# Kernel tuning notes

Hardware: AMD Instinct MI355X
Metric: run time of the kernel (lower is better)

## Reference

```python
import jax, jax.numpy as jnp
import numpy as np

TEMPERATURE = 8.0  # sqrt(head_dim=64)


def setup_inputs() -> dict:
    key = jax.random.key(0)
    kq, kk, kv, km = jax.random.split(key, 4)
    B, S, D = 16, 2048, 64
    q = jax.random.normal(kq, (B, S, D), dtype=jnp.float32)
    k = jax.random.normal(kk, (B, S, D), dtype=jnp.float32)
    v = jax.random.normal(kv, (B, S, D), dtype=jnp.float32)
    mask = jax.random.randint(km, (B, S, S), 0, 2).astype(jnp.bool_)
    return {"q": q, "k": k, "v": v, "mask": mask}


def reference(q, k, v, mask):
    # latent = q @ k^T / temperature  -> [B, Sq, Sk]
    latent = jnp.einsum('bqd,bkd->bqk', q, k) / TEMPERATURE
    # NOTE: the original fills masked positions with 1e-9 (NOT -inf); keep faithful.
    latent = jnp.where(mask, jnp.float32(1e-9), latent)
    attn = jax.nn.softmax(latent, axis=-1)
    return jnp.einsum('bqk,bkd->bqd', attn, v)
```

## Files before the change

kernel.cpp:

```cpp
#include <hip/hip_runtime.h>
#include <hip/hip_bf16.h>

#define BB 16
#define SS 2048
#define DD 64

typedef __attribute__((ext_vector_type(8)))  unsigned short ushort8;
typedef __attribute__((ext_vector_type(8)))  __bf16 bf16x8;
typedef __attribute__((ext_vector_type(16))) float f32x16;

static __device__ __forceinline__ unsigned short f2bf(float x) {
    return __builtin_bit_cast(unsigned short, __float2bfloat16(x));
}
static __device__ __forceinline__ unsigned pk2(float a, float b) {
    return (unsigned)f2bf(a) | ((unsigned)f2bf(b) << 16);
}
union F4 { float4 v; float a[4]; };

__global__ __launch_bounds__(256, 4)
void sdpa_mfma_kernel(const float* __restrict__ Q, const float* __restrict__ K,
                      const float* __restrict__ V, const unsigned int* __restrict__ M,
                      float* __restrict__ O) {
    __shared__ __align__(16) char smem[37120];
    char* Ks = smem;
    char* Vs = smem + 16384;
    char* Ms = smem + 32768;
    char* Qs = smem + 32768;
    float* red  = (float*)smem;
    float* denx = (float*)(smem + 32768);

    const int t    = threadIdx.x;
    const int lane = t & 63;
    const int l31  = lane & 31;
    const int half = lane >> 5;
    const int kh   = t >> 6;
    const int b    = blockIdx.y;
    const int q0   = blockIdx.x * 32;

    const float* Kg = K + (size_t)b * SS * DD;
    const float* Vg = V + (size_t)b * SS * DD;
    const unsigned int* Mg = M + (size_t)b * SS * SS + (size_t)q0 * SS;

    {
        const int sr = t >> 3, sc = t & 7;
        const float* src = Q + ((size_t)b * SS + q0 + sr) * DD + sc * 8;
        F4 f0, f1; f0.v = *(const float4*)src; f1.v = *(const float4*)(src + 4);
        ushort8 u;
        #pragma unroll
        for (int e = 0; e < 4; e++) {
            u[e]     = f2bf(f0.a[e] * 0.125f);
            u[e + 4] = f2bf(f1.a[e] * 0.125f);
        }
        *(ushort8*)(Qs + sr * 128 + ((sc ^ (sr & 7)) * 16)) = u;
    }
    __syncthreads();

    const int qrow = l31;
    bf16x8 bq[4];
    #pragma unroll
    for (int dc = 0; dc < 4; dc++)
        bq[dc] = __builtin_bit_cast(bf16x8, *(const ushort8*)(
            Qs + qrow * 128 + (((2 * dc + half) ^ (qrow & 7)) * 16)));
    __syncthreads();

    f32x16 On0, On1;
    #pragma unroll
    for (int i = 0; i < 16; i++) { On0[i] = 0.f; On1[i] = 0.f; }
    float den_acc = 0.f;

    const int krow = 32 * kh + l31;
    const int d0v  = (t & 15) * 4;
    const int kkb  = (t >> 4) * 4;

    for (int kt = 0; kt < SS / 128; ++kt) {
        #pragma unroll
        for (int j = 0; j < 4; j++) {
            const int idx = 2 * t + 512 * j;
            const int row = idx >> 4;
            const int g   = (idx & 15) >> 1;
            const float* src = Kg + (size_t)(kt * 128) * DD + (size_t)idx * 4;
            F4 fa, fb; fa.v = *(const float4*)src; fb.v = *(const float4*)(src + 4);
            ushort8 u;
            #pragma unroll
            for (int e = 0; e < 4; e++) { u[e] = f2bf(fa.a[e]); u[e + 4] = f2bf(fb.a[e]); }
            *(ushort8*)(Ks + row * 128 + ((g ^ (row & 7)) * 16)) = u;
        }
        #pragma unroll
        for (int it2 = 0; it2 < 2; it2++) {
            const int kk = kkb + 64 * it2;
            const float* src = Vg + (size_t)(kt * 128 + kk) * DD + d0v;
            F4 r0, r1, r2, r3;
            r0.v = *(const float4*)(src);
            r1.v = *(const float4*)(src + DD);
            r2.v = *(const float4*)(src + 2 * DD);
            r3.v = *(const float4*)(src + 3 * DD);
            #pragma unroll
            for (int e = 0; e < 4; e++) {
                const int d = d0v + e;
                const uint2 wv = make_uint2(pk2(r0.a[e], r1.a[e]), pk2(r2.a[e], r3.a[e]));
                *(uint2*)(Vs + d * 256 + (((kk >> 3) ^ (d & 15)) * 16) + (kk & 7) * 2) = wv;
            }
        }
        {
            const int sr = t >> 3, sc = t & 7;
            const unsigned int* Mw = Mg + (size_t)sr * SS + kt * 128 + sc * 16;
            unsigned wd[4];
            #pragma unroll
            for (int g = 0; g < 4; g++) {
                const uint4 u = *(const uint4*)(Mw + 4 * g);
                wd[g] = (u.x ? 1u : 0u) | (u.y ? 0x100u : 0u) |
                        (u.z ? 0x10000u : 0u) | (u.w ? 0x1000000u : 0u);
            }
            *(uint2*)(Ms + sr * 136 + sc * 16)     = make_uint2(wd[0], wd[1]);
            *(uint2*)(Ms + sr * 136 + sc * 16 + 8) = make_uint2(wd[2], wd[3]);
        }
        __syncthreads();

        f32x16 S;
        #pragma unroll
        for (int i = 0; i < 16; i++) S[i] = 0.f;
        #pragma unroll
        for (int dc = 0; dc < 4; dc++) {
            bf16x8 ak = __builtin_bit_cast(bf16x8, *(const ushort8*)(
                Ks + krow * 128 + (((2 * dc + half) ^ (krow & 7)) * 16)));
            S = __builtin_amdgcn_mfma_f32_32x32x16_bf16(ak, bq[dc], S, 0, 0, 0);
        }

        float p[16];
        #pragma unroll
        for (int g = 0; g < 4; g++) {
            const unsigned mw = *(const unsigned*)(Ms + qrow * 136 + 32 * kh + 8 * g + 4 * half);
            #pragma unroll
            for (int e = 0; e < 4; e++) {
                const float ev = __expf(S[4 * g + e]);
                const float pv = ((mw >> (8 * e)) & 0xffu) ? 1.0f : ev;
                p[4 * g + e] = pv;
                den_acc += pv;
            }
        }

        #pragma unroll
        for (int s2 = 0; s2 < 2; s2++) {
            const unsigned o0 = pk2(p[8 * s2 + 0], p[8 * s2 + 1]);
            const unsigned o1 = pk2(p[8 * s2 + 2], p[8 * s2 + 3]);
            const unsigned o2 = pk2(p[8 * s2 + 4], p[8 * s2 + 5]);
            const unsigned o3 = pk2(p[8 * s2 + 6], p[8 * s2 + 7]);
            const unsigned s0 = half ? o0 : o2;
            const unsigned s1 = half ? o1 : o3;
            const unsigned r0 = (unsigned)__shfl_xor((int)s0, 32, 64);
            const unsigned r1 = (unsigned)__shfl_xor((int)s1, 32, 64);
            uint4 bu;
            bu.x = half ? r0 : o0;
            bu.y = half ? r1 : o1;
            bu.z = half ? o2 : r0;
            bu.w = half ? o3 : r1;
            const bf16x8 bp = __builtin_bit_cast(bf16x8, bu);
            #pragma unroll
            for (int dc = 0; dc < 2; dc++) {
                const int vrow = 32 * dc + l31;
                bf16x8 av = __builtin_bit_cast(bf16x8, *(const ushort8*)(
                    Vs + vrow * 256 + (((4 * kh + 2 * s2 + half) ^ (vrow & 15)) * 16)));
                if (dc == 0) On0 = __builtin_amdgcn_mfma_f32_32x32x16_bf16(av, bp, On0, 0, 0, 0);
                else         On1 = __builtin_amdgcn_mfma_f32_32x32x16_bf16(av, bp, On1, 0, 0, 0);
            }
        }
        __syncthreads();
    }

    const float den_tot = den_acc + __shfl_xor(den_acc, 32, 64);

    __syncthreads();
    if (kh != 0) {
        #pragma unroll
        for (int dc = 0; dc < 2; dc++)
            #pragma unroll
            for (int g = 0; g < 4; g++) {
                const f32x16& Oc = dc ? On1 : On0;
                float4 st;
                st.x = Oc[4 * g + 0]; st.y = Oc[4 * g + 1];
                st.z = Oc[4 * g + 2]; st.w = Oc[4 * g + 3];
                *(float4*)((char*)red + (kh - 1) * 8192 + (dc * 4 + g) * 1024 + lane * 16) = st;
            }
        if (lane < 32) denx[kh * 32 + l31] = den_tot;
    }
    __syncthreads();
    if (kh == 0) {
        const float inv = 1.0f / (den_tot + denx[32 + l31] + denx[64 + l31] + denx[96 + l31]);
        float* Og = O + ((size_t)b * SS + q0 + qrow) * DD;
        #pragma unroll
        for (int dc = 0; dc < 2; dc++)
            #pragma unroll
            for (int g = 0; g < 4; g++) {
                const f32x16& Oc = dc ? On1 : On0;
                float4 st;
                st.x = Oc[4 * g + 0]; st.y = Oc[4 * g + 1];
                st.z = Oc[4 * g + 2]; st.w = Oc[4 * g + 3];
                #pragma unroll
                for (int w2 = 0; w2 < 3; w2++) {
                    const float4 pr = *(const float4*)((char*)red + w2 * 8192 +
                                                       (dc * 4 + g) * 1024 + lane * 16);
                    st.x += pr.x; st.y += pr.y; st.z += pr.z; st.w += pr.w;
                }
                st.x *= inv; st.y *= inv; st.z *= inv; st.w *= inv;
                *(float4*)(Og + 32 * dc + 8 * g + 4 * half) = st;
            }
    }
}

extern "C" void kernel_launch(void* const* d_in, const int* in_sizes, int n_in,
                              void* d_out, int out_size, void* d_ws, size_t ws_size,
                              hipStream_t stream) {
    const float* q = (const float*)d_in[0];
    const float* k = (const float*)d_in[1];
    const float* v = (const float*)d_in[2];
    const unsigned int* m = (const unsigned int*)d_in[3];
    float* out = (float*)d_out;

    dim3 grid(SS / 32, BB);
    sdpa_mfma_kernel<<<grid, 256, 0, stream>>>(q, k, v, m, out);
}
```

Before: 394.4 us.

## Prepack the whole mask block into a bitmask before the key loop

The mask for the block's 32 query rows is now streamed once up front, with a one-row-ahead register prefetch, and compressed into a 1-bit-per-key table in shared memory. The per-tile mask staging and byte-packing inside the key loop are removed, and each lane reads a single 32-bit word per tile. This takes mask traffic out of the main loop's critical path and shrinks the per-tile shared-memory footprint. The cost is a serialized prologue of 32 dependent row loads, slightly more shared memory (40 KB), which may reduce occupancy, and the removal of a barrier before the reduction scratch reuses shared memory.

```diff
diff --git a/kernel.cpp b/kernel.cpp
--- a/kernel.cpp
+++ b/kernel.cpp
@@ -4,6 +4,7 @@
 #define BB 16
 #define SS 2048
 #define DD 64
+#define NTB 16
 
 typedef __attribute__((ext_vector_type(8)))  unsigned short ushort8;
 typedef __attribute__((ext_vector_type(8)))  __bf16 bf16x8;
@@ -21,13 +22,11 @@
 void sdpa_mfma_kernel(const float* __restrict__ Q, const float* __restrict__ K,
                       const float* __restrict__ V, const unsigned int* __restrict__ M,
                       float* __restrict__ O) {
-    __shared__ __align__(16) char smem[37120];
-    char* Ks = smem;
-    char* Vs = smem + 16384;
-    char* Ms = smem + 32768;
-    char* Qs = smem + 32768;
-    float* red  = (float*)smem;
-    float* denx = (float*)(smem + 32768);
+    __shared__ __align__(16) char smem[40960];
+    char* Ks   = smem;
+    char* Vs   = smem + 16384;
+    char* Qs   = smem + 32768;
+    char* Bits = smem + 32768;
 
     const int t    = threadIdx.x;
     const int lane = t & 63;
@@ -39,7 +38,12 @@
 
     const float* Kg = K + (size_t)b * SS * DD;
     const float* Vg = V + (size_t)b * SS * DD;
-    const unsigned int* Mg = M + (size_t)b * SS * SS + (size_t)q0 * SS;
+    const unsigned int* Mblk = M + (size_t)b * SS * SS + (size_t)q0 * SS;
+
+    const int kw  = t >> 2;
+    const int bsh = 8 * (t & 3);
+    uint4 c0 = *(const uint4*)(Mblk + 8 * t);
+    uint4 c1 = *(const uint4*)(Mblk + 8 * t + 4);
 
     {
         const int sr = t >> 3, sc = t & 7;
@@ -63,6 +67,23 @@
             Qs + qrow * 128 + (((2 * dc + half) ^ (qrow & 7)) * 16)));
     __syncthreads();
 
+    for (int s = 0; s < 32; ++s) {
+        const int sn = (s + 1 < 32) ? s + 1 : 31;
+        const uint4 n0 = *(const uint4*)(Mblk + (size_t)sn * SS + 8 * t);
+        const uint4 n1 = *(const uint4*)(Mblk + (size_t)sn * SS + 8 * t + 4);
+        unsigned byt = (unsigned)(c0.x != 0u)        | ((unsigned)(c0.y != 0u) << 1)
+                     | ((unsigned)(c0.z != 0u) << 2) | ((unsigned)(c0.w != 0u) << 3)
+                     | ((unsigned)(c1.x != 0u) << 4) | ((unsigned)(c1.y != 0u) << 5)
+                     | ((unsigned)(c1.z != 0u) << 6) | ((unsigned)(c1.w != 0u) << 7);
+        unsigned v = byt << bsh;
+        v |= (unsigned)__shfl_xor((int)v, 1, 64);
+        v |= (unsigned)__shfl_xor((int)v, 2, 64);
+        if ((t & 3) == 0)
+            *(unsigned*)(Bits + kw * 128 + (((s + kw) & 31) << 2)) = v;
+        c0 = n0; c1 = n1;
+    }
+    __syncthreads();
+
     f32x16 On0, On1;
     #pragma unroll
     for (int i = 0; i < 16; i++) { On0[i] = 0.f; On1[i] = 0.f; }
@@ -70,9 +91,9 @@
 
     const int krow = 32 * kh + l31;
     const int d0v  = (t & 15) * 4;
-    const int kkb  = (t >> 4) * 4;
-
-    for (int kt = 0; kt < SS / 128; ++kt) {
+    const int kk4  = (t >> 4) * 4;
+
+    for (int kt = 0; kt < NTB; ++kt) {
         #pragma unroll
         for (int j = 0; j < 4; j++) {
             const int idx = 2 * t + 512 * j;
@@ -87,7 +108,7 @@
         }
         #pragma unroll
         for (int it2 = 0; it2 < 2; it2++) {
-            const int kk = kkb + 64 * it2;
+            const int kk = kk4 + 64 * it2;
             const float* src = Vg + (size_t)(kt * 128 + kk) * DD + d0v;
             F4 r0, r1, r2, r3;
             r0.v = *(const float4*)(src);
@@ -97,22 +118,9 @@
             #pragma unroll
             for (int e = 0; e < 4; e++) {
                 const int d = d0v + e;
-                const uint2 wv = make_uint2(pk2(r0.a[e], r1.a[e]), pk2(r2.a[e], r3.a[e]));
-                *(uint2*)(Vs + d * 256 + (((kk >> 3) ^ (d & 15)) * 16) + (kk & 7) * 2) = wv;
-            }
-        }
-        {
-            const int sr = t >> 3, sc = t & 7;
-            const unsigned int* Mw = Mg + (size_t)sr * SS + kt * 128 + sc * 16;
-            unsigned wd[4];
-            #pragma unroll
-            for (int g = 0; g < 4; g++) {
-                const uint4 u = *(const uint4*)(Mw + 4 * g);
-                wd[g] = (u.x ? 1u : 0u) | (u.y ? 0x100u : 0u) |
-                        (u.z ? 0x10000u : 0u) | (u.w ? 0x1000000u : 0u);
-            }
-            *(uint2*)(Ms + sr * 136 + sc * 16)     = make_uint2(wd[0], wd[1]);
-            *(uint2*)(Ms + sr * 136 + sc * 16 + 8) = make_uint2(wd[2], wd[3]);
+                *(uint2*)(Vs + d * 256 + (((kk >> 3) ^ (d & 15)) * 16) + (kk & 7) * 2)
+                    = make_uint2(pk2(r0.a[e], r1.a[e]), pk2(r2.a[e], r3.a[e]));
+            }
         }
         __syncthreads();
 
@@ -126,14 +134,16 @@
             S = __builtin_amdgcn_mfma_f32_32x32x16_bf16(ak, bq[dc], S, 0, 0, 0);
         }
 
+        const int kwi = 4 * kt + kh;
+        const unsigned bitw = *(const unsigned*)(Bits + kwi * 128 +
+                                  (((l31 + kwi) & 31) << 2));
         float p[16];
         #pragma unroll
         for (int g = 0; g < 4; g++) {
-            const unsigned mw = *(const unsigned*)(Ms + qrow * 136 + 32 * kh + 8 * g + 4 * half);
             #pragma unroll
             for (int e = 0; e < 4; e++) {
                 const float ev = __expf(S[4 * g + e]);
-                const float pv = ((mw >> (8 * e)) & 0xffu) ? 1.0f : ev;
+                const float pv = ((bitw >> (4 * half + 8 * g + e)) & 1u) ? 1.0f : ev;
                 p[4 * g + e] = pv;
                 den_acc += pv;
             }
@@ -156,20 +166,21 @@
             bu.w = half ? o3 : r1;
             const bf16x8 bp = __builtin_bit_cast(bf16x8, bu);
             #pragma unroll
-            for (int dc = 0; dc < 2; dc++) {
-                const int vrow = 32 * dc + l31;
+            for (int dc2 = 0; dc2 < 2; dc2++) {
+                const int vrow = 32 * dc2 + l31;
                 bf16x8 av = __builtin_bit_cast(bf16x8, *(const ushort8*)(
                     Vs + vrow * 256 + (((4 * kh + 2 * s2 + half) ^ (vrow & 15)) * 16)));
-                if (dc == 0) On0 = __builtin_amdgcn_mfma_f32_32x32x16_bf16(av, bp, On0, 0, 0, 0);
-                else         On1 = __builtin_amdgcn_mfma_f32_32x32x16_bf16(av, bp, On1, 0, 0, 0);
+                if (dc2 == 0) On0 = __builtin_amdgcn_mfma_f32_32x32x16_bf16(av, bp, On0, 0, 0, 0);
+                else          On1 = __builtin_amdgcn_mfma_f32_32x32x16_bf16(av, bp, On1, 0, 0, 0);
             }
         }
         __syncthreads();
     }
 
     const float den_tot = den_acc + __shfl_xor(den_acc, 32, 64);
-
-    __syncthreads();
+    float* red  = (float*)smem;
+    float* denx = (float*)(smem + 24576);
+
     if (kh != 0) {
         #pragma unroll
         for (int dc = 0; dc < 2; dc++)
```

Result: slower. 444.5 us (+12.7%).
